# Kernel optimization log

Measured on AMD Instinct MI355X. Metric: run time of the kernel, lower is better.

Reference implementation:

```python
import jax, jax.numpy as jnp
import numpy as np

D_MODEL = 1024
D_INNER = 2048
N_EXPERTS = 8
TOP_K = 2
INIT_STD = 0.02


def setup_inputs() -> dict:
    key = jax.random.key(0)
    ks = jax.random.split(key, 6)
    B, S = 2, 2048
    x = jax.random.normal(ks[0], (B, S, D_MODEL), dtype=jnp.float32)
    router_w = jax.random.normal(ks[1], (N_EXPERTS, D_MODEL), dtype=jnp.float32) * (INIT_STD * 0.1)
    router_b = jnp.zeros((N_EXPERTS,), dtype=jnp.float32)
    gate_w = jax.random.normal(ks[2], (N_EXPERTS, D_MODEL, D_INNER), dtype=jnp.float32) * INIT_STD
    up_w = jax.random.normal(ks[3], (N_EXPERTS, D_MODEL, D_INNER), dtype=jnp.float32) * INIT_STD
    down_w = jax.random.normal(ks[4], (N_EXPERTS, D_INNER, D_MODEL), dtype=jnp.float32) * INIT_STD
    return {"x": x, "router_w": router_w, "router_b": router_b,
            "gate_w": gate_w, "up_w": up_w, "down_w": down_w}


def reference(x, router_w, router_b, gate_w, up_w, down_w):
    # Router: softmax over experts, top-k, renormalize top-k probs.
    logits = jnp.einsum('bsd,ed->bse', x, router_w) + router_b          # [B,S,E]
    probs = jax.nn.softmax(logits, axis=-1)
    top_p, top_i = jax.lax.top_k(probs, TOP_K)                           # [B,S,K]
    top_p = top_p / jnp.sum(top_p, axis=-1, keepdims=True)
    # Per-expert combine weight: c[b,s,e] = sum_k top_p[b,s,k] * [top_i[b,s,k]==e]
    onehot = jax.nn.one_hot(top_i, N_EXPERTS, dtype=x.dtype)             # [B,S,K,E]
    combine = jnp.einsum('bsk,bske->bse', top_p, onehot)                 # [B,S,E]
    # SwiGLU FFN for every expert (dense form of the masked dispatch),
    # zeroed/weighted by combine coefficients.
    g = jnp.einsum('bsd,edf->ebsf', x, gate_w)                           # [E,B,S,F]
    u = jnp.einsum('bsd,edf->ebsf', x, up_w)
    h = jax.nn.silu(g) * u
    y = jnp.einsum('ebsf,efd->ebsd', h, down_w)                          # [E,B,S,D]
    out = jnp.einsum('ebsd,bse->bsd', y, combine)
    return out
```

## Files before the change

kernel.cpp:

```cpp
#include <hip/hip_runtime.h>
#include <hip/hip_bf16.h>
#include <stdint.h>

#define D_MODEL 1024
#define D_INNER 2048
#define NEXP 8
#define TOPK 2
#define BM 128
#define MAXT 72

typedef float f32x4 __attribute__((ext_vector_type(4)));
typedef short bf16x8 __attribute__((ext_vector_type(8)));

__device__ __forceinline__ unsigned short f2b(float f) {
    union { float f; uint32_t u; } v; v.f = f;
    uint32_t u = v.u;
    return (unsigned short)((u + 0x7fffu + ((u >> 16) & 1u)) >> 16);
}

__device__ __forceinline__ void gl_lds16(const void* g, void* l) {
    __builtin_amdgcn_global_load_lds((const __attribute__((address_space(1))) void*)g,
                                     (__attribute__((address_space(3))) void*)l, 16, 0, 0);
}

__global__ __launch_bounds__(256) void cast_x_kernel(
    const float* __restrict__ in, unsigned short* __restrict__ out, int n8)
{
    int i = blockIdx.x * 256 + threadIdx.x;
    if (i >= n8) return;
    const float4* p = (const float4*)(in + (size_t)i * 8);
    float4 a = p[0], b = p[1];
    unsigned short o[8] = {f2b(a.x), f2b(a.y), f2b(a.z), f2b(a.w),
                           f2b(b.x), f2b(b.y), f2b(b.z), f2b(b.w)};
    *(uint4*)(out + (size_t)i * 8) = *(uint4*)o;
}

__global__ __launch_bounds__(256) void tcast_kernel(
    const float* __restrict__ in, unsigned short* __restrict__ out, int K, int N)
{
    __shared__ unsigned short S[64][68];
    int e = blockIdx.z;
    int n0 = blockIdx.x * 64, k0 = blockIdx.y * 64;
    const float* ib = in + (size_t)e * K * N;
    unsigned short* ob = out + (size_t)e * N * K;
    int tid = threadIdx.x;
    int kk = tid >> 4, nn4 = (tid & 15) * 4;
#pragma unroll
    for (int j = 0; j < 4; j++) {
        int k = kk + 16 * j;
        float4 v = *(const float4*)&ib[(size_t)(k0 + k) * N + n0 + nn4];
        ushort4 s; s.x = f2b(v.x); s.y = f2b(v.y); s.z = f2b(v.z); s.w = f2b(v.w);
        *(ushort4*)&S[k][nn4] = s;
    }
    __syncthreads();
    int nn = tid >> 4, kk4 = (tid & 15) * 4;
#pragma unroll
    for (int j = 0; j < 4; j++) {
        int n = nn + 16 * j;
        ushort4 s;
        s.x = S[kk4 + 0][n]; s.y = S[kk4 + 1][n];
        s.z = S[kk4 + 2][n]; s.w = S[kk4 + 3][n];
        *(ushort4*)&ob[(size_t)(n0 + n) * K + k0 + kk4] = s;
    }
}

__global__ __launch_bounds__(64) void router_kernel(
    const float* __restrict__ x, const float* __restrict__ rw,
    const float* __restrict__ rb, int* __restrict__ top_i,
    float* __restrict__ top_w, int T)
{
    int t = blockIdx.x;
    if (t >= T) return;
    int l = threadIdx.x;
    float xv[16];
#pragma unroll
    for (int i = 0; i < 16; i++) xv[i] = x[(size_t)t * D_MODEL + l + 64 * i];
    float logit[NEXP];
#pragma unroll
    for (int e = 0; e < NEXP; e++) {
        float acc = 0.f;
#pragma unroll
        for (int i = 0; i < 16; i++) acc += xv[i] * rw[e * D_MODEL + l + 64 * i];
#pragma unroll
        for (int s = 32; s > 0; s >>= 1) acc += __shfl_xor(acc, s, 64);
        logit[e] = acc + rb[e];
    }
    if (l == 0) {
        int i0 = 0; float m0 = logit[0];
#pragma unroll
        for (int e = 1; e < NEXP; e++) if (logit[e] > m0) { m0 = logit[e]; i0 = e; }
        int i1 = -1; float m1 = -3.0e38f;
#pragma unroll
        for (int e = 0; e < NEXP; e++) {
            if (e == i0) continue;
            if (logit[e] > m1) { m1 = logit[e]; i1 = e; }
        }
        float w0 = 1.f / (1.f + expf(m1 - m0));
        top_i[t * 2 + 0] = i0; top_i[t * 2 + 1] = i1;
        top_w[t * 2 + 0] = w0; top_w[t * 2 + 1] = 1.f - w0;
    }
}

__global__ __launch_bounds__(256) void bucket_kernel(
    const int* __restrict__ top_i, const float* __restrict__ top_w,
    int* __restrict__ meta, int* __restrict__ tok_of_slot,
    float* __restrict__ w_of_slot, int T)
{
    __shared__ int cnt[256][NEXP];
    __shared__ int pre[256][NEXP];
    __shared__ int tot[NEXP];
    __shared__ int off[NEXP + 1];
    int tid = threadIdx.x;
    int per = (T + 255) / 256;
    int t0 = tid * per;
    for (int e = 0; e < NEXP; e++) cnt[tid][e] = 0;
    for (int t = t0; t < t0 + per && t < T; t++)
        for (int k = 0; k < TOPK; k++) cnt[tid][top_i[t * 2 + k]]++;
    __syncthreads();
    if (tid < NEXP) {
        int run = 0;
        for (int i = 0; i < 256; i++) { pre[i][tid] = run; run += cnt[i][tid]; }
        tot[tid] = run;
    }
    __syncthreads();
    if (tid == 0) {
        off[0] = 0;
        for (int e = 0; e < NEXP; e++) off[e + 1] = off[e] + tot[e];
        for (int e = 0; e <= NEXP; e++) meta[e] = off[e];
        int nt = 0;
        for (int e = 0; e < NEXP; e++)
            for (int r = off[e]; r < off[e + 1]; r += BM)
                meta[16 + nt++] = (e << 16) | r;
        for (; nt < MAXT; nt++) meta[16 + nt] = -1;
    }
    __syncthreads();
    int lc[NEXP];
#pragma unroll
    for (int e = 0; e < NEXP; e++) lc[e] = 0;
    for (int t = t0; t < t0 + per && t < T; t++) {
        for (int k = 0; k < TOPK; k++) {
            int e = top_i[t * 2 + k];
            int slot = off[e] + pre[tid][e] + lc[e]++;
            tok_of_slot[slot] = t;
            w_of_slot[slot] = top_w[t * 2 + k];
        }
    }
}

__global__ __launch_bounds__(256, 2) void moe_gate_up(
    const unsigned short* __restrict__ xb, const unsigned short* __restrict__ wgT,
    const unsigned short* __restrict__ wuT, const int* __restrict__ meta,
    const int* __restrict__ tok_of_slot, unsigned short* __restrict__ H)
{
    __shared__ unsigned short As[2][BM * 64];
    __shared__ unsigned short Bg[2][64 * 64];
    __shared__ unsigned short Bu[2][64 * 64];

    int lin = blockIdx.x;
    int xcd = lin & 7, idx = lin >> 3;
    int tix = idx >> 2;
    int f0 = (xcd * 4 + (idx & 3)) * 64;
    int packed = meta[16 + tix];
    if (packed < 0) return;
    int e = packed >> 16, row0 = packed & 0xffff;
    int Mloc = min(BM, meta[e + 1] - row0);

    int tid = threadIdx.x, wv = tid >> 6, lane = tid & 63;
    int l3 = lane >> 3, c3 = lane & 7;

    const unsigned short* srcA[4];
#pragma unroll
    for (int j = 0; j < 4; j++) {
        int r = wv * 32 + j * 8 + l3;
        int slot = row0 + ((r < Mloc) ? r : 0);
        int tok = tok_of_slot[slot];
        srcA[j] = xb + (size_t)tok * D_MODEL + 8 * (c3 ^ (r & 7));
    }
    const unsigned short* srcG[2]; const unsigned short* srcU[2];
#pragma unroll
    for (int j = 0; j < 2; j++) {
        int r = wv * 16 + j * 8 + l3;
        size_t off = (size_t)e * D_MODEL * D_INNER + (size_t)(f0 + r) * D_MODEL + 8 * (c3 ^ (r & 7));
        srcG[j] = wgT + off; srcU[j] = wuT + off;
    }

    int wm = wv >> 1, wn = wv & 1;
    int lrow = lane & 15, kgrp = lane >> 4;
    int swz = lrow & 7;

    f32x4 accg[4][2], accu[4][2];
#pragma unroll
    for (int i = 0; i < 4; i++)
#pragma unroll
        for (int j = 0; j < 2; j++) {
            accg[i][j] = (f32x4){0.f, 0.f, 0.f, 0.f};
            accu[i][j] = (f32x4){0.f, 0.f, 0.f, 0.f};
        }

    int arow[4], brow[2];
#pragma unroll
    for (int fm = 0; fm < 4; fm++) arow[fm] = (wm * 64 + fm * 16 + lrow) * 64;
#pragma unroll
    for (int fn = 0; fn < 2; fn++) brow[fn] = (wn * 32 + fn * 16 + lrow) * 64;

#pragma unroll
    for (int j = 0; j < 4; j++) gl_lds16(srcA[j], As[0] + (wv * 256 + j * 64) * 8);
#pragma unroll
    for (int j = 0; j < 2; j++) {
        gl_lds16(srcG[j], Bg[0] + (wv * 128 + j * 64) * 8);
        gl_lds16(srcU[j], Bu[0] + (wv * 128 + j * 64) * 8);
    }
    __syncthreads();

    int cur = 0;
    for (int k0 = 0; k0 < D_MODEL; k0 += 64, cur ^= 1) {
        if (k0 + 64 < D_MODEL) {
            int nxt = cur ^ 1, kn = k0 + 64;
#pragma unroll
            for (int j = 0; j < 4; j++) gl_lds16(srcA[j] + kn, As[nxt] + (wv * 256 + j * 64) * 8);
#pragma unroll
            for (int j = 0; j < 2; j++) {
                gl_lds16(srcG[j] + kn, Bg[nxt] + (wv * 128 + j * 64) * 8);
                gl_lds16(srcU[j] + kn, Bu[nxt] + (wv * 128 + j * 64) * 8);
            }
        }
        const unsigned short* Ac = As[cur];
        const unsigned short* Gc = Bg[cur];
        const unsigned short* Uc = Bu[cur];
#pragma unroll
        for (int ks = 0; ks < 2; ks++) {
            int co = 8 * ((4 * ks + kgrp) ^ swz);
            bf16x8 a[4], bg[2], bu[2];
#pragma unroll
            for (int fm = 0; fm < 4; fm++) a[fm] = *(const bf16x8*)&Ac[arow[fm] + co];
#pragma unroll
            for (int fn = 0; fn < 2; fn++) {
                bg[fn] = *(const bf16x8*)&Gc[brow[fn] + co];
                bu[fn] = *(const bf16x8*)&Uc[brow[fn] + co];
            }
#pragma unroll
            for (int fm = 0; fm < 4; fm++)
#pragma unroll
                for (int fn = 0; fn < 2; fn++) {
                    accg[fm][fn] = __builtin_amdgcn_mfma_f32_16x16x32_bf16(a[fm], bg[fn], accg[fm][fn], 0, 0, 0);
                    accu[fm][fn] = __builtin_amdgcn_mfma_f32_16x16x32_bf16(a[fm], bu[fn], accu[fm][fn], 0, 0, 0);
                }
        }
        __syncthreads();
    }

#pragma unroll
    for (int fm = 0; fm < 4; fm++)
#pragma unroll
        for (int fn = 0; fn < 2; fn++)
#pragma unroll
            for (int r = 0; r < 4; r++) {
                int m = wm * 64 + fm * 16 + kgrp * 4 + r;
                if (m < Mloc) {
                    int n = wn * 32 + fn * 16 + lrow;
                    float g = accg[fm][fn][r], u = accu[fm][fn][r];
                    float h = g / (1.f + __expf(-g)) * u;
                    H[(size_t)(row0 + m) * D_INNER + f0 + n] = f2b(h);
                }
            }
}

__global__ __launch_bounds__(256, 2) void moe_down(
    const unsigned short* __restrict__ H, const unsigned short* __restrict__ wdT,
    const int* __restrict__ meta, const int* __restrict__ tok_of_slot,
    const float* __restrict__ w_of_slot, float* __restrict__ out, int S2)
{
    __shared__ unsigned short As[2][BM * 64];
    __shared__ unsigned short Bs[2][BM * 64];
    __shared__ int toks[BM];
    __shared__ float wts[BM];

    int lin = blockIdx.x;
    int d0 = (lin & 7) * BM;
    int tix = lin >> 3;
    int packed = meta[16 + tix];
    if (packed < 0) return;
    int e = packed >> 16, row0 = packed & 0xffff;
    int Mloc = min(BM, meta[e + 1] - row0);

    int tid = threadIdx.x, wv = tid >> 6, lane = tid & 63;
    int l3 = lane >> 3, c3 = lane & 7;
    if (tid < BM) {
        bool v = tid < Mloc;
        toks[tid] = v ? tok_of_slot[row0 + tid] : 0;
        wts[tid] = v ? w_of_slot[row0 + tid] : 0.f;
    }

    const unsigned short* srcA[4]; const unsigned short* srcB[4];
#pragma unroll
    for (int j = 0; j < 4; j++) {
        int r = wv * 32 + j * 8 + l3;
        int slot = min(row0 + r, S2 - 1);
        srcA[j] = H + (size_t)slot * D_INNER + 8 * (c3 ^ (r & 7));
        srcB[j] = wdT + (size_t)e * D_INNER * D_MODEL + (size_t)(d0 + r) * D_INNER + 8 * (c3 ^ (r & 7));
    }

    int wm = wv >> 1, wn = wv & 1;
    int lrow = lane & 15, kgrp = lane >> 4;
    int swz = lrow & 7;

    f32x4 acc[4][4];
#pragma unroll
    for (int i = 0; i < 4; i++)
#pragma unroll
        for (int j = 0; j < 4; j++) acc[i][j] = (f32x4){0.f, 0.f, 0.f, 0.f};

    int arow[4], brow[4];
#pragma unroll
    for (int fm = 0; fm < 4; fm++) arow[fm] = (wm * 64 + fm * 16 + lrow) * 64;
#pragma unroll
    for (int fn = 0; fn < 4; fn++) brow[fn] = (wn * 64 + fn * 16 + lrow) * 64;

#pragma unroll
    for (int j = 0; j < 4; j++) {
        gl_lds16(srcA[j], As[0] + (wv * 256 + j * 64) * 8);
        gl_lds16(srcB[j], Bs[0] + (wv * 256 + j * 64) * 8);
    }
    __syncthreads();

    int cur = 0;
    for (int k0 = 0; k0 < D_INNER; k0 += 64, cur ^= 1) {
        if (k0 + 64 < D_INNER) {
            int nxt = cur ^ 1, kn = k0 + 64;
#pragma unroll
            for (int j = 0; j < 4; j++) {
                gl_lds16(srcA[j] + kn, As[nxt] + (wv * 256 + j * 64) * 8);
                gl_lds16(srcB[j] + kn, Bs[nxt] + (wv * 256 + j * 64) * 8);
            }
        }
        const unsigned short* Ac = As[cur];
        const unsigned short* Bc = Bs[cur];
#pragma unroll
        for (int ks = 0; ks < 2; ks++) {
            int co = 8 * ((4 * ks + kgrp) ^ swz);
            bf16x8 a[4], b[4];
#pragma unroll
            for (int fm = 0; fm < 4; fm++) a[fm] = *(const bf16x8*)&Ac[arow[fm] + co];
#pragma unroll
            for (int fn = 0; fn < 4; fn++) b[fn] = *(const bf16x8*)&Bc[brow[fn] + co];
#pragma unroll
            for (int fm = 0; fm < 4; fm++)
#pragma unroll
                for (int fn = 0; fn < 4; fn++)
                    acc[fm][fn] = __builtin_amdgcn_mfma_f32_16x16x32_bf16(a[fm], b[fn], acc[fm][fn], 0, 0, 0);
        }
        __syncthreads();
    }

#pragma unroll
    for (int fm = 0; fm < 4; fm++)
#pragma unroll
        for (int fn = 0; fn < 4; fn++)
#pragma unroll
            for (int r = 0; r < 4; r++) {
                int m = wm * 64 + fm * 16 + kgrp * 4 + r;
                if (m < Mloc) {
                    int n = wn * 64 + fn * 16 + lrow;
                    atomicAdd(&out[(size_t)toks[m] * D_MODEL + d0 + n], wts[m] * acc[fm][fn][r]);
                }
            }
}

extern "C" void kernel_launch(void* const* d_in, const int* in_sizes, int n_in,
                              void* d_out, int out_size, void* d_ws, size_t ws_size,
                              hipStream_t stream) {
    const float* x  = (const float*)d_in[0];
    const float* rw = (const float*)d_in[1];
    const float* rb = (const float*)d_in[2];
    const float* gw = (const float*)d_in[3];
    const float* uw = (const float*)d_in[4];
    const float* dw = (const float*)d_in[5];
    float* out = (float*)d_out;

    int T = in_sizes[0] / D_MODEL;
    int S2 = 2 * T;

    char* ws = (char*)d_ws;
    size_t cur = 0;
    auto take = [&](size_t bytes) { char* p = ws + cur; cur = (cur + bytes + 255) & ~(size_t)255; return p; };
    int*   top_i = (int*)take((size_t)S2 * 4);
    float* top_w = (float*)take((size_t)S2 * 4);
    int*   meta  = (int*)take(1024);
    int*   tos   = (int*)take((size_t)S2 * 4);
    float* wos   = (float*)take((size_t)S2 * 4);
    unsigned short* xb  = (unsigned short*)take((size_t)T * D_MODEL * 2);
    unsigned short* wgT = (unsigned short*)take((size_t)NEXP * D_MODEL * D_INNER * 2);
    unsigned short* wuT = (unsigned short*)take((size_t)NEXP * D_MODEL * D_INNER * 2);
    unsigned short* wdT = (unsigned short*)take((size_t)NEXP * D_MODEL * D_INNER * 2);
    unsigned short* H   = (unsigned short*)take((size_t)S2 * D_INNER * 2);

    hipMemsetAsync(d_out, 0, (size_t)out_size * sizeof(float), stream);

    int n8 = T * D_MODEL / 8;
    cast_x_kernel<<<(n8 + 255) / 256, 256, 0, stream>>>(x, xb, n8);
    tcast_kernel<<<dim3(D_INNER / 64, D_MODEL / 64, NEXP), 256, 0, stream>>>(gw, wgT, D_MODEL, D_INNER);
    tcast_kernel<<<dim3(D_INNER / 64, D_MODEL / 64, NEXP), 256, 0, stream>>>(uw, wuT, D_MODEL, D_INNER);
    tcast_kernel<<<dim3(D_MODEL / 64, D_INNER / 64, NEXP), 256, 0, stream>>>(dw, wdT, D_INNER, D_MODEL);

    router_kernel<<<T, 64, 0, stream>>>(x, rw, rb, top_i, top_w, T);
    bucket_kernel<<<1, 256, 0, stream>>>(top_i, top_w, meta, tos, wos, T);

    moe_gate_up<<<MAXT * 32, 256, 0, stream>>>(xb, wgT, wuT, meta, tos, H);
    moe_down<<<MAXT * 8, 256, 0, stream>>>(H, wdT, meta, tos, wos, out, S2);
}
```

Before: 303.6 us.

## Use partial vmcnt waits and raw barriers to keep prefetch in flight

Replaces __syncthreads in both grouped GEMM loops with explicit s_waitcnt vmcnt(8) plus s_barrier, so the next tile's global-to-LDS loads stay outstanding while the current tile is consumed. It also raises wave priority around the MFMA block with s_setprio. This removes the full vmcnt(0) drain that __syncthreads forces at each iteration. The hand-written waitcnt counts depend on exactly 8 loads per thread being issued per stage, and a wrong count risks reading incomplete LDS data.

New measurement: 293.8 us. 3.2% less time.

```diff
diff --git a/kernel.cpp b/kernel.cpp
--- a/kernel.cpp
+++ b/kernel.cpp
@@ -11,6 +11,8 @@
 
 typedef float f32x4 __attribute__((ext_vector_type(4)));
 typedef short bf16x8 __attribute__((ext_vector_type(8)));
+
+#define MEMFENCE asm volatile("" ::: "memory")
 
 __device__ __forceinline__ unsigned short f2b(float f) {
     union { float f; uint32_t u; } v; v.f = f;
@@ -210,11 +212,12 @@
         gl_lds16(srcG[j], Bg[0] + (wv * 128 + j * 64) * 8);
         gl_lds16(srcU[j], Bu[0] + (wv * 128 + j * 64) * 8);
     }
-    __syncthreads();
+    MEMFENCE;
 
     int cur = 0;
     for (int k0 = 0; k0 < D_MODEL; k0 += 64, cur ^= 1) {
-        if (k0 + 64 < D_MODEL) {
+        bool more = (k0 + 64 < D_MODEL);
+        if (more) {
             int nxt = cur ^ 1, kn = k0 + 64;
 #pragma unroll
             for (int j = 0; j < 4; j++) gl_lds16(srcA[j] + kn, As[nxt] + (wv * 256 + j * 64) * 8);
@@ -223,10 +226,17 @@
                 gl_lds16(srcG[j] + kn, Bg[nxt] + (wv * 128 + j * 64) * 8);
                 gl_lds16(srcU[j] + kn, Bu[nxt] + (wv * 128 + j * 64) * 8);
             }
-        }
+            asm volatile("s_waitcnt vmcnt(8)" ::: "memory");
+        } else {
+            asm volatile("s_waitcnt vmcnt(0)" ::: "memory");
+        }
+        __builtin_amdgcn_s_barrier();
+        MEMFENCE;
+
         const unsigned short* Ac = As[cur];
         const unsigned short* Gc = Bg[cur];
         const unsigned short* Uc = Bu[cur];
+        __builtin_amdgcn_s_setprio(1);
 #pragma unroll
         for (int ks = 0; ks < 2; ks++) {
             int co = 8 * ((4 * ks + kgrp) ^ swz);
@@ -236,7 +246,7 @@
 #pragma unroll
             for (int fn = 0; fn < 2; fn++) {
                 bg[fn] = *(const bf16x8*)&Gc[brow[fn] + co];
-                bu[fn] = *(const bf16x8*)&Uc[brow[fn] + co];
+                bu[fn] = *(const bf16x8*)&Bu[cur][brow[fn] + co];
             }
 #pragma unroll
             for (int fm = 0; fm < 4; fm++)
@@ -246,7 +256,12 @@
                     accu[fm][fn] = __builtin_amdgcn_mfma_f32_16x16x32_bf16(a[fm], bu[fn], accu[fm][fn], 0, 0, 0);
                 }
         }
-        __syncthreads();
+        __builtin_amdgcn_s_setprio(0);
+        MEMFENCE;
+        asm volatile("s_waitcnt lgkmcnt(0)" ::: "memory");
+        __builtin_amdgcn_s_barrier();
+        MEMFENCE;
+        (void)Uc;
     }
 
 #pragma unroll
@@ -321,20 +336,28 @@
         gl_lds16(srcA[j], As[0] + (wv * 256 + j * 64) * 8);
         gl_lds16(srcB[j], Bs[0] + (wv * 256 + j * 64) * 8);
     }
-    __syncthreads();
+    MEMFENCE;
 
     int cur = 0;
     for (int k0 = 0; k0 < D_INNER; k0 += 64, cur ^= 1) {
-        if (k0 + 64 < D_INNER) {
+        bool more = (k0 + 64 < D_INNER);
+        if (more) {
             int nxt = cur ^ 1, kn = k0 + 64;
 #pragma unroll
             for (int j = 0; j < 4; j++) {
                 gl_lds16(srcA[j] + kn, As[nxt] + (wv * 256 + j * 64) * 8);
                 gl_lds16(srcB[j] + kn, Bs[nxt] + (wv * 256 + j * 64) * 8);
             }
-        }
+            asm volatile("s_waitcnt vmcnt(8)" ::: "memory");
+        } else {
+            asm volatile("s_waitcnt vmcnt(0)" ::: "memory");
+        }
+        __builtin_amdgcn_s_barrier();
+        MEMFENCE;
+
         const unsigned short* Ac = As[cur];
         const unsigned short* Bc = Bs[cur];
+        __builtin_amdgcn_s_setprio(1);
 #pragma unroll
         for (int ks = 0; ks < 2; ks++) {
             int co = 8 * ((4 * ks + kgrp) ^ swz);
@@ -349,7 +372,11 @@
                 for (int fn = 0; fn < 4; fn++)
                     acc[fm][fn] = __builtin_amdgcn_mfma_f32_16x16x32_bf16(a[fm], b[fn], acc[fm][fn], 0, 0, 0);
         }
-        __syncthreads();
+        __builtin_amdgcn_s_setprio(0);
+        MEMFENCE;
+        asm volatile("s_waitcnt lgkmcnt(0)" ::: "memory");
+        __builtin_amdgcn_s_barrier();
+        MEMFENCE;
     }
 
 #pragma unroll
```
